# Kernel optimization log

Measured on AMD Instinct MI355X. Metric: run time of the kernel, lower is better.

The kernel has to match this reference:

```python
import jax, jax.numpy as jnp
import numpy as np

D_MODEL = 512
NUM_HEADS = 8
D_QKV = D_MODEL // NUM_HEADS  # 64
CAPACITY = 2  # EUNN tunable-style rotation layers per step
B = 2
L = 256


def setup_inputs() -> dict:
    key = jax.random.key(0)
    ks = jax.random.split(key, 16)
    f = jnp.float32
    x_q = jax.random.normal(ks[0], (B, L, D_MODEL), f)
    x_k = jax.random.normal(ks[1], (B, L, D_MODEL), f)
    x_v = jax.random.normal(ks[2], (B, L, D_MODEL), f)
    mask = jnp.zeros((B, 1, L, L), f)
    s = 1.0 / np.sqrt(D_MODEL).astype(np.float32)
    Wq = jax.random.normal(ks[3], (D_MODEL, D_MODEL), f) * s
    Wk = jax.random.normal(ks[4], (D_MODEL, D_MODEL), f) * s
    Wv = jax.random.normal(ks[5], (D_MODEL, D_MODEL), f) * s
    Wo = jax.random.normal(ks[6], (D_MODEL, D_MODEL), f) * s
    bq = jnp.zeros((D_MODEL,), f); bk = jnp.zeros((D_MODEL,), f)
    bv = jnp.zeros((D_MODEL,), f); bo = jnp.zeros((D_MODEL,), f)
    pi = np.float32(np.pi)
    theta = jax.random.uniform(ks[7], (NUM_HEADS, CAPACITY, D_QKV // 2), f, -pi, pi)
    phi = jax.random.uniform(ks[8], (NUM_HEADS, CAPACITY, D_QKV // 2), f, -pi, pi)
    sw = 1.0 / np.sqrt(D_QKV).astype(np.float32)
    Win_re = jax.random.normal(ks[9], (NUM_HEADS, D_QKV, D_QKV), f) * sw
    Win_im = jax.random.normal(ks[10], (NUM_HEADS, D_QKV, D_QKV), f) * sw
    rnn_bias = jax.random.normal(ks[11], (NUM_HEADS, D_QKV), f) * 0.01
    return dict(x_q=x_q, x_k=x_k, x_v=x_v, mask=mask, Wq=Wq, bq=bq, Wk=Wk, bk=bk,
                Wv=Wv, bv=bv, Wo=Wo, bo=bo, theta=theta, phi=phi,
                Win_re=Win_re, Win_im=Win_im, rnn_bias=rnn_bias)


def _apply_unitary(h, theta, phi):
    # h: [B,H,Q,d] complex64. EUNN unitary = product of Givens-rotation layers,
    # alternating even pairings (0,1),(2,3),.. and odd pairings via roll.
    for c in range(theta.shape[1]):
        if c % 2 == 1:
            h = jnp.roll(h, -1, axis=-1)
        sh = h.shape
        hp = h.reshape(sh[:-1] + (sh[-1] // 2, 2))
        a, b = hp[..., 0], hp[..., 1]
        cs = jnp.cos(theta[:, c, :])[None, :, None, :]
        sn = jnpp_sin = jnp.sin(theta[:, c, :])[None, :, None, :]
        ph = jnp.exp(1j * phi[:, c, :].astype(jnp.complex64))[None, :, None, :]
        na = cs * a - (sn * ph) * b
        nb = (sn * jnp.conj(ph)) * a + cs * b
        h = jnp.stack([na, nb], axis=-1).reshape(sh)
        if c % 2 == 1:
            h = jnp.roll(h, 1, axis=-1)
    return h


def _modrelu(z, b):
    m = jnp.abs(z)
    scale = jax.nn.relu(m + b) / (m + 1e-5)
    return z * scale.astype(z.dtype)


def _forward(x_q, x_k, x_v, mask, Wq, bq, Wk, bk, Wv, bv, Wo, bo,
             theta, phi, Win_re, Win_im, rnn_bias):
    Bm, Lq, _ = x_q.shape
    def heads(x):
        return x.reshape(Bm, -1, NUM_HEADS, D_QKV).transpose(0, 2, 1, 3)
    q = heads(x_q @ Wq + bq)   # [B,H,Lq,d]
    k = heads(x_k @ Wk + bk)   # [B,H,Lk,d]
    v = heads(x_v @ Wv + bv)   # [B,H,Lk,d]
    logits = jnp.einsum('bhqd,bhkd->bhqk', q, k) / jnp.sqrt(jnp.float32(D_QKV))
    logits = logits - jnp.where(mask == 1.0, jnp.inf, mask)
    attn = jax.nn.softmax(logits, axis=-1)  # [B,H,Lq,Lk]
    Win = (Win_re + 1j * Win_im).astype(jnp.complex64)  # [H,d,d]
    bb = rnn_bias[None, :, None, :]
    def step(h, xs):
        a_t, v_t = xs                              # [B,H,Q], [B,H,d]
        x_t = a_t[..., None] * v_t[:, :, None, :]  # [B,H,Q,d] streamed weighted value
        wx = jnp.einsum('bhqd,hde->bhqe', x_t.astype(jnp.complex64), Win)
        return _modrelu(_apply_unitary(h, theta, phi) + wx, bb), None
    h0 = jnp.zeros((Bm, NUM_HEADS, Lq, D_QKV), jnp.complex64)
    xs = (attn.transpose(3, 0, 1, 2), v.transpose(2, 0, 1, 3))
    hT, _ = jax.lax.scan(step, h0, xs)
    rnn_out = jnp.real(hT)  # [B,H,Lq,d] -- TF takes final RNN state, real part
    out = rnn_out.transpose(0, 2, 1, 3).reshape(Bm, Lq, D_MODEL) @ Wo + bo
    return out, attn


def reference(x_q, x_k, x_v, mask, Wq, bq, Wk, bk, Wv, bv, Wo, bo,
              theta, phi, Win_re, Win_im, rnn_bias):
    return _forward(x_q, x_k, x_v, mask, Wq, bq, Wk, bk, Wv, bv, Wo, bo,
                    theta, phi, Win_re, Win_im, rnn_bias)
```

## Files before the change

### kernel.cpp

```cpp
#include <hip/hip_runtime.h>
#include <math.h>

#define NB 2
#define NL 256
#define DM 512
#define NH 8
#define DQ 64

__global__ __launch_bounds__(256) void qkv_gemm(
    const float* __restrict__ xq, const float* __restrict__ xk,
    const float* __restrict__ xv,
    const float* __restrict__ Wq, const float* __restrict__ Wk,
    const float* __restrict__ Wv,
    const float* __restrict__ bq, const float* __restrict__ bk,
    const float* __restrict__ bv,
    float* __restrict__ q, float* __restrict__ k, float* __restrict__ v)
{
    int z = blockIdx.z;
    const float* X = (z == 0) ? xq : (z == 1) ? xk : xv;
    const float* W = (z == 0) ? Wq : (z == 1) ? Wk : Wv;
    const float* bias = (z == 0) ? bq : (z == 1) ? bk : bv;
    float* O = (z == 0) ? q : (z == 1) ? k : v;

    __shared__ float As[32][33];
    __shared__ float Bs[32][68];

    int tid = threadIdx.x;
    int tx = tid & 15, ty = tid >> 4;
    int m0 = blockIdx.y * 32, n0 = blockIdx.x * 64;

    float acc[2][4] = {};

    for (int k0 = 0; k0 < 512; k0 += 32) {
        {
            int r = tid >> 3, c4 = (tid & 7) * 4;
            const float4 av = *(const float4*)(X + (m0 + r) * 512 + k0 + c4);
            As[c4 + 0][r] = av.x; As[c4 + 1][r] = av.y;
            As[c4 + 2][r] = av.z; As[c4 + 3][r] = av.w;
        }
        {
            int r = tid >> 4, c4 = (tid & 15) * 4;
            float4 b0 = *(const float4*)(W + (k0 + r) * 512 + n0 + c4);
            float4 b1 = *(const float4*)(W + (k0 + r + 16) * 512 + n0 + c4);
            *(float4*)&Bs[r][c4] = b0;
            *(float4*)&Bs[r + 16][c4] = b1;
        }
        __syncthreads();
        #pragma unroll
        for (int kk = 0; kk < 32; kk++) {
            float a0 = As[kk][ty * 2 + 0];
            float a1 = As[kk][ty * 2 + 1];
            float4 bb = *(const float4*)&Bs[kk][tx * 4];
            acc[0][0] += a0 * bb.x; acc[0][1] += a0 * bb.y;
            acc[0][2] += a0 * bb.z; acc[0][3] += a0 * bb.w;
            acc[1][0] += a1 * bb.x; acc[1][1] += a1 * bb.y;
            acc[1][2] += a1 * bb.z; acc[1][3] += a1 * bb.w;
        }
        __syncthreads();
    }

    #pragma unroll
    for (int i = 0; i < 2; i++) {
        int m = m0 + ty * 2 + i;
        int b = m >> 8, l = m & 255;
        #pragma unroll
        for (int j = 0; j < 4; j++) {
            int n = n0 + tx * 4 + j;
            int h = n >> 6, d = n & 63;
            O[((b * NH + h) * NL + l) * DQ + d] = acc[i][j] + bias[n];
        }
    }
}

__global__ __launch_bounds__(256) void attn_u_kernel(
    const float* __restrict__ q, const float* __restrict__ k,
    const float* __restrict__ mask, float* __restrict__ attn_o,
    const float* __restrict__ v, const float* __restrict__ Wre,
    const float* __restrict__ Wim, float2* __restrict__ u)
{
    int h = blockIdx.y, b = blockIdx.z;
    int tid = threadIdx.x;
    __shared__ float smem[264];

    if (blockIdx.x < 256) {
        int qi = blockIdx.x;
        int wv = tid >> 6, lane = tid & 63;
        float* qrow = smem;
        float* wred = smem + 256;
        float* wsum = smem + 260;

        if (tid < 16)
            ((float4*)qrow)[tid] = ((const float4*)(q + ((b * NH + h) * NL + qi) * DQ))[tid];
        __syncthreads();

        const float4* kp = (const float4*)(k + ((b * NH + h) * NL + tid) * DQ);
        float acc = 0.f;
        #pragma unroll
        for (int d4 = 0; d4 < 16; d4++) {
            float4 kv = kp[d4];
            float4 qv = ((const float4*)qrow)[d4];
            acc += qv.x * kv.x + qv.y * kv.y + qv.z * kv.z + qv.w * kv.w;
        }
        acc *= 0.125f;

        float mv = mask[(b * NL + qi) * NL + tid];
        acc -= (mv == 1.0f) ? INFINITY : mv;

        float mx = acc;
        #pragma unroll
        for (int o = 32; o; o >>= 1) mx = fmaxf(mx, __shfl_xor(mx, o, 64));
        if (lane == 0) wred[wv] = mx;
        __syncthreads();
        mx = fmaxf(fmaxf(wred[0], wred[1]), fmaxf(wred[2], wred[3]));

        float e = __expf(acc - mx);
        float s = e;
        #pragma unroll
        for (int o = 32; o; o >>= 1) s += __shfl_xor(s, o, 64);
        if (lane == 0) wsum[wv] = s;
        __syncthreads();
        s = wsum[0] + wsum[1] + wsum[2] + wsum[3];

        attn_o[((b * NH + h) * NL + qi) * NL + tid] = e * __builtin_amdgcn_rcpf(s);
    } else {
        int xi = blockIdx.x - 256;
        int e = tid & 63, tq = tid >> 6;
        int t = xi * 4 + tq;
        float (*vrow)[64] = (float (*)[64])smem;

        const float* vp = v + ((b * NH + h) * NL + t) * DQ;
        vrow[tq][e] = vp[e];
        __syncthreads();

        const float* wr = Wre + h * 4096 + e;
        const float* wi = Wim + h * 4096 + e;
        float ar = 0.f, ai = 0.f;
        #pragma unroll
        for (int d = 0; d < 64; d++) {
            float vv = vrow[tq][d];
            ar += vv * wr[d * 64];
            ai += vv * wi[d * 64];
        }
        u[((b * NH + h) * NL + t) * DQ + e] = make_float2(ar, ai);
    }
}

__device__ __forceinline__ float rot_up2(float x) {
    int v = __builtin_amdgcn_mov_dpp(__float_as_int(x), 0x134, 0xF, 0xF, true);
    v = __builtin_amdgcn_mov_dpp(v, 0x134, 0xF, 0xF, true);
    return __int_as_float(v);
}
__device__ __forceinline__ float rot_dn2(float x) {
    int v = __builtin_amdgcn_mov_dpp(__float_as_int(x), 0x13C, 0xF, 0xF, true);
    v = __builtin_amdgcn_mov_dpp(v, 0x13C, 0xF, 0xF, true);
    return __int_as_float(v);
}

__global__ __launch_bounds__(256) void rnn_kernel(
    const float* __restrict__ attn_f, const float2* __restrict__ u,
    const float* __restrict__ theta, const float* __restrict__ phi,
    const float* __restrict__ rnn_bias, float* __restrict__ rnn_out)
{
    int tid = threadIdx.x;
    int wv = tid >> 6;
    int lane = tid & 63;
    int par = lane & 1;
    int p = lane >> 1;
    int rec = blockIdx.x * 8 + wv * 2 + par;
    int qi = rec & 255, h = (rec >> 8) & 7, b = rec >> 11;

    const float* tb = theta + h * 64;
    const float* pb = phi + h * 64;

    float th0 = tb[p], ph0 = pb[p];
    float c0 = cosf(th0), s0 = sinf(th0);
    float cp0 = cosf(ph0), sp0 = sinf(ph0);
    float W0ar = -s0 * cp0, W0ai = -s0 * sp0;
    float W0br =  s0 * cp0, W0bi = -s0 * sp0;

    float th1 = tb[32 + p], ph1 = pb[32 + p];
    float c1 = cosf(th1), s1 = sinf(th1);
    float W1ar = -s1 * cosf(ph1), W1ai = -s1 * sinf(ph1);

    int pm = (p + 31) & 31;
    float th1m = tb[32 + pm], ph1m = pb[32 + pm];
    float c1m = cosf(th1m), s1m = sinf(th1m);
    float W1br = s1m * cosf(ph1m), W1bi = -s1m * sinf(ph1m);

    float bias0 = rnn_bias[h * 64 + 2 * p];
    float bias1 = rnn_bias[h * 64 + 2 * p + 1];

    __shared__ float arow[8 * 256];
    {
        const float4* ap = (const float4*)(attn_f + (size_t)blockIdx.x * 8 * 256);
        ((float4*)arow)[tid] = ap[tid];
        ((float4*)arow)[tid + 256] = ap[tid + 256];
    }
    __syncthreads();
    const float* arc = arow + (wv * 2 + par) * 256;

    const float4* up4 = (const float4*)(u + (size_t)((b * NH + h) * NL) * DQ) + p;

    float e0r = 0.f, e0i = 0.f, e1r = 0.f, e1i = 0.f;
    #pragma unroll 8
    for (int t = 0; t < 256; t++) {
        float4 uu = up4[t * 32];
        float a_t = arc[t];

        float na_r = c0 * e0r + (W0ar * e1r - W0ai * e1i);
        float na_i = c0 * e0i + (W0ar * e1i + W0ai * e1r);
        float nb_r = c0 * e1r + (W0br * e0r - W0bi * e0i);
        float nb_i = c0 * e1i + (W0br * e0i + W0bi * e0r);

        float f1r = rot_up2(na_r), f1i = rot_up2(na_i);
        float f2r = rot_dn2(nb_r), f2i = rot_dn2(nb_i);

        float z1r = c1 * nb_r + (W1ar * f1r - W1ai * f1i);
        float z1i = c1 * nb_i + (W1ar * f1i + W1ai * f1r);
        float z0r = c1m * na_r + (W1br * f2r - W1bi * f2i);
        float z0i = c1m * na_i + (W1br * f2i + W1bi * f2r);

        z0r += a_t * uu.x; z0i += a_t * uu.y;
        z1r += a_t * uu.z; z1i += a_t * uu.w;

        float mm0 = z0r * z0r + z0i * z0i;
        float m0 = __builtin_amdgcn_sqrtf(mm0);
        float sc0 = fmaxf(m0 + bias0, 0.f) * __builtin_amdgcn_rcpf(m0 + 1e-5f);
        e0r = z0r * sc0; e0i = z0i * sc0;

        float mm1 = z1r * z1r + z1i * z1i;
        float m1 = __builtin_amdgcn_sqrtf(mm1);
        float sc1 = fmaxf(m1 + bias1, 0.f) * __builtin_amdgcn_rcpf(m1 + 1e-5f);
        e1r = z1r * sc1; e1i = z1i * sc1;
    }

    float2 o = make_float2(e0r, e1r);
    *(float2*)&rnn_out[(size_t)(b * NL + qi) * DM + h * DQ + 2 * p] = o;
}

__global__ __launch_bounds__(256) void out_gemm(
    const float* __restrict__ A, const float* __restrict__ W,
    const float* __restrict__ bias, float* __restrict__ C)
{
    __shared__ float As[32][17];
    __shared__ float Bs[32][68];

    int tid = threadIdx.x;
    int tx = tid & 15, ty = tid >> 4;
    int m0 = blockIdx.y * 16, n0 = blockIdx.x * 64;

    float acc[4] = {};

    for (int k0 = 0; k0 < 512; k0 += 32) {
        {
            int r = tid >> 4, c2 = (tid & 15) * 2;
            const float2 av = *(const float2*)(A + (m0 + r) * 512 + k0 + c2);
            As[c2 + 0][r] = av.x; As[c2 + 1][r] = av.y;
        }
        {
            int r = tid >> 4, c4 = (tid & 15) * 4;
            float4 b0 = *(const float4*)(W + (k0 + r) * 512 + n0 + c4);
            float4 b1 = *(const float4*)(W + (k0 + r + 16) * 512 + n0 + c4);
            *(float4*)&Bs[r][c4] = b0;
            *(float4*)&Bs[r + 16][c4] = b1;
        }
        __syncthreads();
        #pragma unroll
        for (int kk = 0; kk < 32; kk++) {
            float a = As[kk][ty];
            float4 bb = *(const float4*)&Bs[kk][tx * 4];
            acc[0] += a * bb.x; acc[1] += a * bb.y;
            acc[2] += a * bb.z; acc[3] += a * bb.w;
        }
        __syncthreads();
    }

    int m = m0 + ty;
    #pragma unroll
    for (int j = 0; j < 4; j++) {
        int n = n0 + tx * 4 + j;
        C[m * 512 + n] = acc[j] + bias[n];
    }
}

extern "C" void kernel_launch(void* const* d_in, const int* in_sizes, int n_in,
                              void* d_out, int out_size, void* d_ws, size_t ws_size,
                              hipStream_t stream)
{
    const float* x_q  = (const float*)d_in[0];
    const float* x_k  = (const float*)d_in[1];
    const float* x_v  = (const float*)d_in[2];
    const float* mask = (const float*)d_in[3];
    const float* Wq   = (const float*)d_in[4];
    const float* bq   = (const float*)d_in[5];
    const float* Wk   = (const float*)d_in[6];
    const float* bk   = (const float*)d_in[7];
    const float* Wv   = (const float*)d_in[8];
    const float* bv   = (const float*)d_in[9];
    const float* Wo   = (const float*)d_in[10];
    const float* bo   = (const float*)d_in[11];
    const float* theta= (const float*)d_in[12];
    const float* phi  = (const float*)d_in[13];
    const float* Wre  = (const float*)d_in[14];
    const float* Wim  = (const float*)d_in[15];
    const float* rb   = (const float*)d_in[16];

    float* ws = (float*)d_ws;
    float*  q_ws    = ws;
    float*  k_ws    = ws + 262144;
    float*  v_ws    = ws + 524288;
    float2* u_ws    = (float2*)(ws + 786432);
    float*  rnn_o   = ws + 1310720;

    float* out_o  = (float*)d_out;
    float* attn_o = out_o + NB * NL * DM;

    qkv_gemm<<<dim3(8, 16, 3), 256, 0, stream>>>(
        x_q, x_k, x_v, Wq, Wk, Wv, bq, bk, bv, q_ws, k_ws, v_ws);

    attn_u_kernel<<<dim3(320, NH, NB), 256, 0, stream>>>(
        q_ws, k_ws, mask, attn_o, v_ws, Wre, Wim, u_ws);

    rnn_kernel<<<dim3(512), 256, 0, stream>>>(
        attn_o, u_ws, theta, phi, rb, rnn_o);

    out_gemm<<<dim3(8, 32), 256, 0, stream>>>(rnn_o, Wo, bo, out_o);
}
```

Before: 218.2 us.

## Fuse all four stages into one persistent kernel with grid barriers

Merges the QKV GEMM, attention/softmax plus input projection, the EUNN recurrence and the output GEMM into a single 512-block persistent kernel, with atomic-counter grid barriers between stages. K is now stored transposed so the score dot products read coalesced along the key index. The output GEMM switches to 32-row tiles, and the attention-row staging in shared memory is padded. This aims to remove launch overhead and inter-kernel gaps. In exchange it adds a memset launch, spin-wait barriers that depend on all 512 blocks being co-resident, and idle blocks in the GEMM phases.

```diff
diff --git a/kernel.cpp b/kernel.cpp
--- a/kernel.cpp
+++ b/kernel.cpp
@@ -6,144 +6,7 @@
 #define DM 512
 #define NH 8
 #define DQ 64
-
-__global__ __launch_bounds__(256) void qkv_gemm(
-    const float* __restrict__ xq, const float* __restrict__ xk,
-    const float* __restrict__ xv,
-    const float* __restrict__ Wq, const float* __restrict__ Wk,
-    const float* __restrict__ Wv,
-    const float* __restrict__ bq, const float* __restrict__ bk,
-    const float* __restrict__ bv,
-    float* __restrict__ q, float* __restrict__ k, float* __restrict__ v)
-{
-    int z = blockIdx.z;
-    const float* X = (z == 0) ? xq : (z == 1) ? xk : xv;
-    const float* W = (z == 0) ? Wq : (z == 1) ? Wk : Wv;
-    const float* bias = (z == 0) ? bq : (z == 1) ? bk : bv;
-    float* O = (z == 0) ? q : (z == 1) ? k : v;
-
-    __shared__ float As[32][33];
-    __shared__ float Bs[32][68];
-
-    int tid = threadIdx.x;
-    int tx = tid & 15, ty = tid >> 4;
-    int m0 = blockIdx.y * 32, n0 = blockIdx.x * 64;
-
-    float acc[2][4] = {};
-
-    for (int k0 = 0; k0 < 512; k0 += 32) {
-        {
-            int r = tid >> 3, c4 = (tid & 7) * 4;
-            const float4 av = *(const float4*)(X + (m0 + r) * 512 + k0 + c4);
-            As[c4 + 0][r] = av.x; As[c4 + 1][r] = av.y;
-            As[c4 + 2][r] = av.z; As[c4 + 3][r] = av.w;
-        }
-        {
-            int r = tid >> 4, c4 = (tid & 15) * 4;
-            float4 b0 = *(const float4*)(W + (k0 + r) * 512 + n0 + c4);
-            float4 b1 = *(const float4*)(W + (k0 + r + 16) * 512 + n0 + c4);
-            *(float4*)&Bs[r][c4] = b0;
-            *(float4*)&Bs[r + 16][c4] = b1;
-        }
-        __syncthreads();
-        #pragma unroll
-        for (int kk = 0; kk < 32; kk++) {
-            float a0 = As[kk][ty * 2 + 0];
-            float a1 = As[kk][ty * 2 + 1];
-            float4 bb = *(const float4*)&Bs[kk][tx * 4];
-            acc[0][0] += a0 * bb.x; acc[0][1] += a0 * bb.y;
-            acc[0][2] += a0 * bb.z; acc[0][3] += a0 * bb.w;
-            acc[1][0] += a1 * bb.x; acc[1][1] += a1 * bb.y;
-            acc[1][2] += a1 * bb.z; acc[1][3] += a1 * bb.w;
-        }
-        __syncthreads();
-    }
-
-    #pragma unroll
-    for (int i = 0; i < 2; i++) {
-        int m = m0 + ty * 2 + i;
-        int b = m >> 8, l = m & 255;
-        #pragma unroll
-        for (int j = 0; j < 4; j++) {
-            int n = n0 + tx * 4 + j;
-            int h = n >> 6, d = n & 63;
-            O[((b * NH + h) * NL + l) * DQ + d] = acc[i][j] + bias[n];
-        }
-    }
-}
-
-__global__ __launch_bounds__(256) void attn_u_kernel(
-    const float* __restrict__ q, const float* __restrict__ k,
-    const float* __restrict__ mask, float* __restrict__ attn_o,
-    const float* __restrict__ v, const float* __restrict__ Wre,
-    const float* __restrict__ Wim, float2* __restrict__ u)
-{
-    int h = blockIdx.y, b = blockIdx.z;
-    int tid = threadIdx.x;
-    __shared__ float smem[264];
-
-    if (blockIdx.x < 256) {
-        int qi = blockIdx.x;
-        int wv = tid >> 6, lane = tid & 63;
-        float* qrow = smem;
-        float* wred = smem + 256;
-        float* wsum = smem + 260;
-
-        if (tid < 16)
-            ((float4*)qrow)[tid] = ((const float4*)(q + ((b * NH + h) * NL + qi) * DQ))[tid];
-        __syncthreads();
-
-        const float4* kp = (const float4*)(k + ((b * NH + h) * NL + tid) * DQ);
-        float acc = 0.f;
-        #pragma unroll
-        for (int d4 = 0; d4 < 16; d4++) {
-            float4 kv = kp[d4];
-            float4 qv = ((const float4*)qrow)[d4];
-            acc += qv.x * kv.x + qv.y * kv.y + qv.z * kv.z + qv.w * kv.w;
-        }
-        acc *= 0.125f;
-
-        float mv = mask[(b * NL + qi) * NL + tid];
-        acc -= (mv == 1.0f) ? INFINITY : mv;
-
-        float mx = acc;
-        #pragma unroll
-        for (int o = 32; o; o >>= 1) mx = fmaxf(mx, __shfl_xor(mx, o, 64));
-        if (lane == 0) wred[wv] = mx;
-        __syncthreads();
-        mx = fmaxf(fmaxf(wred[0], wred[1]), fmaxf(wred[2], wred[3]));
-
-        float e = __expf(acc - mx);
-        float s = e;
-        #pragma unroll
-        for (int o = 32; o; o >>= 1) s += __shfl_xor(s, o, 64);
-        if (lane == 0) wsum[wv] = s;
-        __syncthreads();
-        s = wsum[0] + wsum[1] + wsum[2] + wsum[3];
-
-        attn_o[((b * NH + h) * NL + qi) * NL + tid] = e * __builtin_amdgcn_rcpf(s);
-    } else {
-        int xi = blockIdx.x - 256;
-        int e = tid & 63, tq = tid >> 6;
-        int t = xi * 4 + tq;
-        float (*vrow)[64] = (float (*)[64])smem;
-
-        const float* vp = v + ((b * NH + h) * NL + t) * DQ;
-        vrow[tq][e] = vp[e];
-        __syncthreads();
-
-        const float* wr = Wre + h * 4096 + e;
-        const float* wi = Wim + h * 4096 + e;
-        float ar = 0.f, ai = 0.f;
-        #pragma unroll
-        for (int d = 0; d < 64; d++) {
-            float vv = vrow[tq][d];
-            ar += vv * wr[d * 64];
-            ai += vv * wi[d * 64];
-        }
-        u[((b * NH + h) * NL + t) * DQ + e] = make_float2(ar, ai);
-    }
-}
+#define NBLK 512
 
 __device__ __forceinline__ float rot_up2(float x) {
     int v = __builtin_amdgcn_mov_dpp(__float_as_int(x), 0x134, 0xF, 0xF, true);
@@ -156,130 +19,269 @@
     return __int_as_float(v);
 }
 
-__global__ __launch_bounds__(256) void rnn_kernel(
-    const float* __restrict__ attn_f, const float2* __restrict__ u,
+__device__ __forceinline__ void grid_bar(unsigned* c, unsigned n) {
+    __syncthreads();
+    if (threadIdx.x == 0) {
+        __threadfence();
+        atomicAdd(c, 1u);
+        while (__hip_atomic_load(c, __ATOMIC_RELAXED, __HIP_MEMORY_SCOPE_AGENT) < n)
+            __builtin_amdgcn_s_sleep(2);
+        __threadfence();
+    }
+    __syncthreads();
+}
+
+__global__ __launch_bounds__(256, 2) void fused_kernel(
+    const float* __restrict__ xq, const float* __restrict__ xk,
+    const float* __restrict__ xv, const float* __restrict__ mask,
+    const float* __restrict__ Wq, const float* __restrict__ bq_,
+    const float* __restrict__ Wk, const float* __restrict__ bk_,
+    const float* __restrict__ Wv, const float* __restrict__ bv_,
+    const float* __restrict__ Wo, const float* __restrict__ bo_,
     const float* __restrict__ theta, const float* __restrict__ phi,
-    const float* __restrict__ rnn_bias, float* __restrict__ rnn_out)
+    const float* __restrict__ Wre, const float* __restrict__ Wim,
+    const float* __restrict__ rb,
+    float* qbuf, float* kTbuf, float* vbuf, float2* ubuf,
+    float* rnnbuf, float* outbuf, float* attnbuf, unsigned* bars)
 {
+    __shared__ __align__(16) char smem_pool[17408];
     int tid = threadIdx.x;
-    int wv = tid >> 6;
-    int lane = tid & 63;
-    int par = lane & 1;
-    int p = lane >> 1;
-    int rec = blockIdx.x * 8 + wv * 2 + par;
-    int qi = rec & 255, h = (rec >> 8) & 7, b = rec >> 11;
-
-    const float* tb = theta + h * 64;
-    const float* pb = phi + h * 64;
-
-    float th0 = tb[p], ph0 = pb[p];
-    float c0 = cosf(th0), s0 = sinf(th0);
-    float cp0 = cosf(ph0), sp0 = sinf(ph0);
-    float W0ar = -s0 * cp0, W0ai = -s0 * sp0;
-    float W0br =  s0 * cp0, W0bi = -s0 * sp0;
-
-    float th1 = tb[32 + p], ph1 = pb[32 + p];
-    float c1 = cosf(th1), s1 = sinf(th1);
-    float W1ar = -s1 * cosf(ph1), W1ai = -s1 * sinf(ph1);
-
-    int pm = (p + 31) & 31;
-    float th1m = tb[32 + pm], ph1m = pb[32 + pm];
-    float c1m = cosf(th1m), s1m = sinf(th1m);
-    float W1br = s1m * cosf(ph1m), W1bi = -s1m * sinf(ph1m);
-
-    float bias0 = rnn_bias[h * 64 + 2 * p];
-    float bias1 = rnn_bias[h * 64 + 2 * p + 1];
-
-    __shared__ float arow[8 * 256];
+
     {
-        const float4* ap = (const float4*)(attn_f + (size_t)blockIdx.x * 8 * 256);
-        ((float4*)arow)[tid] = ap[tid];
-        ((float4*)arow)[tid + 256] = ap[tid + 256];
-    }
-    __syncthreads();
-    const float* arc = arow + (wv * 2 + par) * 256;
-
-    const float4* up4 = (const float4*)(u + (size_t)((b * NH + h) * NL) * DQ) + p;
-
-    float e0r = 0.f, e0i = 0.f, e1r = 0.f, e1i = 0.f;
-    #pragma unroll 8
-    for (int t = 0; t < 256; t++) {
-        float4 uu = up4[t * 32];
-        float a_t = arc[t];
-
-        float na_r = c0 * e0r + (W0ar * e1r - W0ai * e1i);
-        float na_i = c0 * e0i + (W0ar * e1i + W0ai * e1r);
-        float nb_r = c0 * e1r + (W0br * e0r - W0bi * e0i);
-        float nb_i = c0 * e1i + (W0br * e0i + W0bi * e0r);
-
-        float f1r = rot_up2(na_r), f1i = rot_up2(na_i);
-        float f2r = rot_dn2(nb_r), f2i = rot_dn2(nb_i);
-
-        float z1r = c1 * nb_r + (W1ar * f1r - W1ai * f1i);
-        float z1i = c1 * nb_i + (W1ar * f1i + W1ai * f1r);
-        float z0r = c1m * na_r + (W1br * f2r - W1bi * f2i);
-        float z0i = c1m * na_i + (W1br * f2i + W1bi * f2r);
-
-        z0r += a_t * uu.x; z0i += a_t * uu.y;
-        z1r += a_t * uu.z; z1i += a_t * uu.w;
-
-        float mm0 = z0r * z0r + z0i * z0i;
-        float m0 = __builtin_amdgcn_sqrtf(mm0);
-        float sc0 = fmaxf(m0 + bias0, 0.f) * __builtin_amdgcn_rcpf(m0 + 1e-5f);
-        e0r = z0r * sc0; e0i = z0i * sc0;
-
-        float mm1 = z1r * z1r + z1i * z1i;
-        float m1 = __builtin_amdgcn_sqrtf(mm1);
-        float sc1 = fmaxf(m1 + bias1, 0.f) * __builtin_amdgcn_rcpf(m1 + 1e-5f);
-        e1r = z1r * sc1; e1i = z1i * sc1;
-    }
-
-    float2 o = make_float2(e0r, e1r);
-    *(float2*)&rnn_out[(size_t)(b * NL + qi) * DM + h * DQ + 2 * p] = o;
-}
-
-__global__ __launch_bounds__(256) void out_gemm(
-    const float* __restrict__ A, const float* __restrict__ W,
-    const float* __restrict__ bias, float* __restrict__ C)
-{
-    __shared__ float As[32][17];
-    __shared__ float Bs[32][68];
-
-    int tid = threadIdx.x;
-    int tx = tid & 15, ty = tid >> 4;
-    int m0 = blockIdx.y * 16, n0 = blockIdx.x * 64;
-
-    float acc[4] = {};
-
-    for (int k0 = 0; k0 < 512; k0 += 32) {
-        {
-            int r = tid >> 4, c2 = (tid & 15) * 2;
-            const float2 av = *(const float2*)(A + (m0 + r) * 512 + k0 + c2);
-            As[c2 + 0][r] = av.x; As[c2 + 1][r] = av.y;
+        int job = blockIdx.x;
+        if (job < 384) {
+            float (*As)[33] = (float (*)[33])smem_pool;
+            float (*Bs)[68] = (float (*)[68])(smem_pool + 4224);
+            int z = job / 128, r1 = job % 128;
+            int mt = r1 >> 3, nt = r1 & 7;
+            const float* X = (z == 0) ? xq : (z == 1) ? xk : xv;
+            const float* W = (z == 0) ? Wq : (z == 1) ? Wk : Wv;
+            const float* bias = (z == 0) ? bq_ : (z == 1) ? bk_ : bv_;
+            float* O = (z == 0) ? qbuf : (z == 1) ? kTbuf : vbuf;
+            int tx = tid & 15, ty = tid >> 4;
+            int m0 = mt * 32, n0 = nt * 64;
+            float acc[2][4] = {};
+            for (int k0 = 0; k0 < 512; k0 += 32) {
+                {
+                    int r = tid >> 3, c4 = (tid & 7) * 4;
+                    float4 av = *(const float4*)(X + (m0 + r) * 512 + k0 + c4);
+                    As[c4 + 0][r] = av.x; As[c4 + 1][r] = av.y;
+                    As[c4 + 2][r] = av.z; As[c4 + 3][r] = av.w;
+                }
+                {
+                    int r = tid >> 4, c4 = (tid & 15) * 4;
+                    float4 b0 = *(const float4*)(W + (k0 + r) * 512 + n0 + c4);
+                    float4 b1 = *(const float4*)(W + (k0 + r + 16) * 512 + n0 + c4);
+                    *(float4*)&Bs[r][c4] = b0;
+                    *(float4*)&Bs[r + 16][c4] = b1;
+                }
+                __syncthreads();
+                #pragma unroll
+                for (int kk = 0; kk < 32; kk++) {
+                    float a0 = As[kk][ty * 2 + 0], a1 = As[kk][ty * 2 + 1];
+                    float4 bb = *(const float4*)&Bs[kk][tx * 4];
+                    acc[0][0] += a0 * bb.x; acc[0][1] += a0 * bb.y;
+                    acc[0][2] += a0 * bb.z; acc[0][3] += a0 * bb.w;
+                    acc[1][0] += a1 * bb.x; acc[1][1] += a1 * bb.y;
+                    acc[1][2] += a1 * bb.z; acc[1][3] += a1 * bb.w;
+                }
+                __syncthreads();
+            }
+            #pragma unroll
+            for (int i = 0; i < 2; i++) {
+                int m = m0 + ty * 2 + i;
+                int bb_ = m >> 8, l = m & 255;
+                #pragma unroll
+                for (int jj = 0; jj < 4; jj++) {
+                    int n = n0 + tx * 4 + jj;
+                    int hh = n >> 6, dd = n & 63;
+                    float val = acc[i][jj] + bias[n];
+                    if (z == 1) O[((bb_ * NH + hh) * DQ + dd) * NL + l] = val;
+                    else        O[((bb_ * NH + hh) * NL + l) * DQ + dd] = val;
+                }
+            }
         }
-        {
-            int r = tid >> 4, c4 = (tid & 15) * 4;
-            float4 b0 = *(const float4*)(W + (k0 + r) * 512 + n0 + c4);
-            float4 b1 = *(const float4*)(W + (k0 + r + 16) * 512 + n0 + c4);
-            *(float4*)&Bs[r][c4] = b0;
-            *(float4*)&Bs[r + 16][c4] = b1;
+    }
+    grid_bar(&bars[0], NBLK);
+
+    {
+        float* sp = (float*)smem_pool;
+        for (int j = blockIdx.x; j < 5120; j += NBLK) {
+            int x = j % 320;
+            int hb = j / 320;
+            int h = hb & 7, b = hb >> 3;
+            if (x < 256) {
+                int qi = x;
+                int wv = tid >> 6, lane = tid & 63;
+                float* qrow = sp; float* wred = sp + 256; float* wsum = sp + 260;
+                if (tid < 16)
+                    ((float4*)qrow)[tid] =
+                        ((const float4*)(qbuf + ((b * NH + h) * NL + qi) * DQ))[tid];
+                __syncthreads();
+                const float* kp = kTbuf + (size_t)((b * NH + h) * DQ) * NL + tid;
+                float acc = 0.f;
+                #pragma unroll
+                for (int d = 0; d < 64; d++) acc += qrow[d] * kp[d * NL];
+                acc *= 0.125f;
+                float mv = mask[(b * NL + qi) * NL + tid];
+                acc -= (mv == 1.0f) ? INFINITY : mv;
+                float mx = acc;
+                #pragma unroll
+                for (int o = 32; o; o >>= 1) mx = fmaxf(mx, __shfl_xor(mx, o, 64));
+                if (lane == 0) wred[wv] = mx;
+                __syncthreads();
+                mx = fmaxf(fmaxf(wred[0], wred[1]), fmaxf(wred[2], wred[3]));
+                float e = __expf(acc - mx);
+                float s = e;
+                #pragma unroll
+                for (int o = 32; o; o >>= 1) s += __shfl_xor(s, o, 64);
+                if (lane == 0) wsum[wv] = s;
+                __syncthreads();
+                s = wsum[0] + wsum[1] + wsum[2] + wsum[3];
+                attnbuf[((b * NH + h) * NL + qi) * NL + tid] =
+                    e * __builtin_amdgcn_rcpf(s);
+            } else {
+                int xi = x - 256;
+                int e = tid & 63, tq = tid >> 6;
+                int t = xi * 4 + tq;
+                float (*vrow)[64] = (float (*)[64])sp;
+                vrow[tq][e] = vbuf[((b * NH + h) * NL + t) * DQ + e];
+                __syncthreads();
+                const float* wr = Wre + h * 4096 + e;
+                const float* wi = Wim + h * 4096 + e;
+                float ar = 0.f, ai = 0.f;
+                #pragma unroll
+                for (int d = 0; d < 64; d++) {
+                    float vv = vrow[tq][d];
+                    ar += vv * wr[d * 64];
+                    ai += vv * wi[d * 64];
+                }
+                ubuf[((b * NH + h) * NL + t) * DQ + e] = make_float2(ar, ai);
+            }
+            __syncthreads();
         }
+    }
+    grid_bar(&bars[1], NBLK);
+
+    {
+        int wv = tid >> 6;
+        int lane = tid & 63;
+        int par = lane & 1;
+        int p = lane >> 1;
+        int rec = blockIdx.x * 8 + wv * 2 + par;
+        int qi = rec & 255, h = (rec >> 8) & 7, b = rec >> 11;
+
+        const float* tb = theta + h * 64;
+        const float* pb = phi + h * 64;
+
+        float th0 = tb[p], ph0 = pb[p];
+        float c0 = cosf(th0), s0 = sinf(th0);
+        float cp0 = cosf(ph0), sp0 = sinf(ph0);
+        float W0ar = -s0 * cp0, W0ai = -s0 * sp0;
+        float W0br =  s0 * cp0, W0bi = -s0 * sp0;
+
+        float th1 = tb[32 + p], ph1 = pb[32 + p];
+        float c1 = cosf(th1), s1v = sinf(th1);
+        float W1ar = -s1v * cosf(ph1), W1ai = -s1v * sinf(ph1);
+
+        int pm = (p + 31) & 31;
+        float th1m = tb[32 + pm], ph1m = pb[32 + pm];
+        float c1m = cosf(th1m), s1m = sinf(th1m);
+        float W1br = s1m * cosf(ph1m), W1bi = -s1m * sinf(ph1m);
+
+        float bias0 = rb[h * 64 + 2 * p];
+        float bias1 = rb[h * 64 + 2 * p + 1];
+
+        float* arow = (float*)smem_pool;
+        const float* ap = attnbuf + (size_t)blockIdx.x * 2048;
+        #pragma unroll
+        for (int i = 0; i < 8; i++) arow[i * 257 + tid] = ap[i * 256 + tid];
         __syncthreads();
-        #pragma unroll
-        for (int kk = 0; kk < 32; kk++) {
-            float a = As[kk][ty];
-            float4 bb = *(const float4*)&Bs[kk][tx * 4];
-            acc[0] += a * bb.x; acc[1] += a * bb.y;
-            acc[2] += a * bb.z; acc[3] += a * bb.w;
+        const float* arc = arow + (wv * 2 + par) * 257;
+
+        const float4* up4 =
+            (const float4*)(ubuf + (size_t)((b * NH + h) * NL) * DQ) + p;
+
+        float e0r = 0.f, e0i = 0.f, e1r = 0.f, e1i = 0.f;
+        #pragma unroll 8
+        for (int t = 0; t < 256; t++) {
+            float4 uu = up4[t * 32];
+            float a_t = arc[t];
+
+            float na_r = c0 * e0r + (W0ar * e1r - W0ai * e1i);
+            float na_i = c0 * e0i + (W0ar * e1i + W0ai * e1r);
+            float nb_r = c0 * e1r + (W0br * e0r - W0bi * e0i);
+            float nb_i = c0 * e1i + (W0br * e0i + W0bi * e0r);
+
+            float f1r = rot_up2(na_r), f1i = rot_up2(na_i);
+            float f2r = rot_dn2(nb_r), f2i = rot_dn2(nb_i);
+
+            float z1r = c1 * nb_r + (W1ar * f1r - W1ai * f1i) + a_t * uu.z;
+            float z1i = c1 * nb_i + (W1ar * f1i + W1ai * f1r) + a_t * uu.w;
+            float z0r = c1m * na_r + (W1br * f2r - W1bi * f2i) + a_t * uu.x;
+            float z0i = c1m * na_i + (W1br * f2i + W1bi * f2r) + a_t * uu.y;
+
+            float mm0 = z0r * z0r + z0i * z0i;
+            float m0v = __builtin_amdgcn_sqrtf(mm0);
+            float sc0 = fmaxf(m0v + bias0, 0.f) * __builtin_amdgcn_rcpf(m0v + 1e-5f);
+            e0r = z0r * sc0; e0i = z0i * sc0;
+
+            float mm1 = z1r * z1r + z1i * z1i;
+            float m1v = __builtin_amdgcn_sqrtf(mm1);
+            float sc1 = fmaxf(m1v + bias1, 0.f) * __builtin_amdgcn_rcpf(m1v + 1e-5f);
+            e1r = z1r * sc1; e1i = z1i * sc1;
         }
-        __syncthreads();
-    }
-
-    int m = m0 + ty;
-    #pragma unroll
-    for (int j = 0; j < 4; j++) {
-        int n = n0 + tx * 4 + j;
-        C[m * 512 + n] = acc[j] + bias[n];
+
+        *(float2*)&rnnbuf[(size_t)(b * NL + qi) * DM + h * DQ + 2 * p] =
+            make_float2(e0r, e1r);
+    }
+    grid_bar(&bars[2], NBLK);
+
+    {
+        int job = blockIdx.x;
+        if (job < 128) {
+            float (*As)[33] = (float (*)[33])smem_pool;
+            float (*Bs)[68] = (float (*)[68])(smem_pool + 4224);
+            int mt = job >> 3, nt = job & 7;
+            int tx = tid & 15, ty = tid >> 4;
+            int m0 = mt * 32, n0 = nt * 64;
+            float acc[2][4] = {};
+            for (int k0 = 0; k0 < 512; k0 += 32) {
+                {
+                    int r = tid >> 3, c4 = (tid & 7) * 4;
+                    float4 av = *(const float4*)(rnnbuf + (m0 + r) * 512 + k0 + c4);
+                    As[c4 + 0][r] = av.x; As[c4 + 1][r] = av.y;
+                    As[c4 + 2][r] = av.z; As[c4 + 3][r] = av.w;
+                }
+                {
+                    int r = tid >> 4, c4 = (tid & 15) * 4;
+                    float4 b0 = *(const float4*)(Wo + (k0 + r) * 512 + n0 + c4);
+                    float4 b1 = *(const float4*)(Wo + (k0 + r + 16) * 512 + n0 + c4);
+                    *(float4*)&Bs[r][c4] = b0;
+                    *(float4*)&Bs[r + 16][c4] = b1;
+                }
+                __syncthreads();
+                #pragma unroll
+                for (int kk = 0; kk < 32; kk++) {
+                    float a0 = As[kk][ty * 2 + 0], a1 = As[kk][ty * 2 + 1];
+                    float4 bb = *(const float4*)&Bs[kk][tx * 4];
+                    acc[0][0] += a0 * bb.x; acc[0][1] += a0 * bb.y;
+                    acc[0][2] += a0 * bb.z; acc[0][3] += a0 * bb.w;
+                    acc[1][0] += a1 * bb.x; acc[1][1] += a1 * bb.y;
+                    acc[1][2] += a1 * bb.z; acc[1][3] += a1 * bb.w;
+                }
+                __syncthreads();
+            }
+            #pragma unroll
+            for (int i = 0; i < 2; i++) {
+                int m = m0 + ty * 2 + i;
+                #pragma unroll
+                for (int jj = 0; jj < 4; jj++) {
+                    int n = n0 + tx * 4 + jj;
+                    outbuf[m * 512 + n] = acc[i][jj] + bo_[n];
+                }
+            }
+        }
     }
 }
 
@@ -306,23 +308,20 @@
     const float* rb   = (const float*)d_in[16];
 
     float* ws = (float*)d_ws;
-    float*  q_ws    = ws;
-    float*  k_ws    = ws + 262144;
-    float*  v_ws    = ws + 524288;
-    float2* u_ws    = (float2*)(ws + 786432);
-    float*  rnn_o   = ws + 1310720;
+    float*    q_ws  = ws;
+    float*    kT_ws = ws + 262144;
+    float*    v_ws  = ws + 524288;
+    float2*   u_ws  = (float2*)(ws + 786432);
+    float*    rnn_o = ws + 1310720;
+    unsigned* bars  = (unsigned*)(ws + 1572864);
 
     float* out_o  = (float*)d_out;
     float* attn_o = out_o + NB * NL * DM;
 
-    qkv_gemm<<<dim3(8, 16, 3), 256, 0, stream>>>(
-        x_q, x_k, x_v, Wq, Wk, Wv, bq, bk, bv, q_ws, k_ws, v_ws);
-
-    attn_u_kernel<<<dim3(320, NH, NB), 256, 0, stream>>>(
-        q_ws, k_ws, mask, attn_o, v_ws, Wre, Wim, u_ws);
-
-    rnn_kernel<<<dim3(512), 256, 0, stream>>>(
-        attn_o, u_ws, theta, phi, rb, rnn_o);
-
-    out_gemm<<<dim3(8, 32), 256, 0, stream>>>(rnn_o, Wo, bo, out_o);
-}
+    hipMemsetAsync(bars, 0, 3 * sizeof(unsigned), stream);
+
+    fused_kernel<<<dim3(NBLK), 256, 0, stream>>>(
+        x_q, x_k, x_v, mask, Wq, bq, Wk, bk, Wv, bv, Wo, bo,
+        theta, phi, Wre, Wim, rb,
+        q_ws, kT_ws, v_ws, u_ws, rnn_o, out_o, attn_o, bars);
+}
```

Measured after the change: 351.5 us. 61.1% more time.

## Store K transposed and compute eight query rows per attention block

Applied to the files above, without the earlier changes.

The QKV GEMM now writes K in a [b,h,d,l] layout, so the attention kernel reads K coalesced across threads. Each attention block now handles 8 query rows instead of one. K loads are reused across those rows, logits are staged in shared memory, and each wave does the softmax reduction for two rows. This cuts block count and redundant K traffic, at the cost of more shared memory, more registers and strided stores in the GEMM epilogue.

```diff
diff --git a/kernel.cpp b/kernel.cpp
--- a/kernel.cpp
+++ b/kernel.cpp
@@ -67,69 +67,86 @@
         for (int j = 0; j < 4; j++) {
             int n = n0 + tx * 4 + j;
             int h = n >> 6, d = n & 63;
-            O[((b * NH + h) * NL + l) * DQ + d] = acc[i][j] + bias[n];
+            float val = acc[i][j] + bias[n];
+            if (z == 1)
+                O[((b * NH + h) * DQ + d) * NL + l] = val;
+            else
+                O[((b * NH + h) * NL + l) * DQ + d] = val;
         }
     }
 }
 
 __global__ __launch_bounds__(256) void attn_u_kernel(
-    const float* __restrict__ q, const float* __restrict__ k,
+    const float* __restrict__ q, const float* __restrict__ kT,
     const float* __restrict__ mask, float* __restrict__ attn_o,
     const float* __restrict__ v, const float* __restrict__ Wre,
     const float* __restrict__ Wim, float2* __restrict__ u)
 {
     int h = blockIdx.y, b = blockIdx.z;
     int tid = threadIdx.x;
-    __shared__ float smem[264];
-
-    if (blockIdx.x < 256) {
-        int qi = blockIdx.x;
+    int x = blockIdx.x;
+    __shared__ float sp[2608];
+
+    if (x < 32) {
+        int qg = x;
         int wv = tid >> 6, lane = tid & 63;
-        float* qrow = smem;
-        float* wred = smem + 256;
-        float* wsum = smem + 260;
-
-        if (tid < 16)
-            ((float4*)qrow)[tid] = ((const float4*)(q + ((b * NH + h) * NL + qi) * DQ))[tid];
-        __syncthreads();
-
-        const float4* kp = (const float4*)(k + ((b * NH + h) * NL + tid) * DQ);
-        float acc = 0.f;
+        float* qs   = sp;
+        float* lg   = sp + 512;
+        float* redm = sp + 512 + 2080;
+        float* reds = redm + 8;
+
+        ((float2*)qs)[tid] =
+            ((const float2*)(q + ((size_t)(b * NH + h) * NL + qg * 8) * DQ))[tid];
+        __syncthreads();
+
+        const float* kp = kT + (size_t)((b * NH + h) * DQ) * NL + tid;
+        float acc[8] = {};
         #pragma unroll
         for (int d4 = 0; d4 < 16; d4++) {
-            float4 kv = kp[d4];
-            float4 qv = ((const float4*)qrow)[d4];
-            acc += qv.x * kv.x + qv.y * kv.y + qv.z * kv.z + qv.w * kv.w;
-        }
-        acc *= 0.125f;
-
-        float mv = mask[(b * NL + qi) * NL + tid];
-        acc -= (mv == 1.0f) ? INFINITY : mv;
-
-        float mx = acc;
-        #pragma unroll
-        for (int o = 32; o; o >>= 1) mx = fmaxf(mx, __shfl_xor(mx, o, 64));
-        if (lane == 0) wred[wv] = mx;
-        __syncthreads();
-        mx = fmaxf(fmaxf(wred[0], wred[1]), fmaxf(wred[2], wred[3]));
-
-        float e = __expf(acc - mx);
-        float s = e;
-        #pragma unroll
-        for (int o = 32; o; o >>= 1) s += __shfl_xor(s, o, 64);
-        if (lane == 0) wsum[wv] = s;
-        __syncthreads();
-        s = wsum[0] + wsum[1] + wsum[2] + wsum[3];
-
-        attn_o[((b * NH + h) * NL + qi) * NL + tid] = e * __builtin_amdgcn_rcpf(s);
+            float kv0 = kp[(d4 * 4 + 0) * NL];
+            float kv1 = kp[(d4 * 4 + 1) * NL];
+            float kv2 = kp[(d4 * 4 + 2) * NL];
+            float kv3 = kp[(d4 * 4 + 3) * NL];
+            #pragma unroll
+            for (int j = 0; j < 8; j++) {
+                const float4 qv = *(const float4*)&qs[j * 64 + d4 * 4];
+                acc[j] += qv.x * kv0 + qv.y * kv1 + qv.z * kv2 + qv.w * kv3;
+            }
+        }
+        #pragma unroll
+        for (int j = 0; j < 8; j++) {
+            float mv = mask[(size_t)(b * NL + qg * 8 + j) * NL + tid];
+            acc[j] = acc[j] * 0.125f - ((mv == 1.0f) ? INFINITY : mv);
+            lg[j * 260 + tid] = acc[j];
+        }
+        __syncthreads();
+        #pragma unroll
+        for (int jj = 0; jj < 2; jj++) {
+            int j = wv * 2 + jj;
+            float v0 = lg[j * 260 + lane],       v1 = lg[j * 260 + 64 + lane];
+            float v2 = lg[j * 260 + 128 + lane], v3 = lg[j * 260 + 192 + lane];
+            float mx = fmaxf(fmaxf(v0, v1), fmaxf(v2, v3));
+            #pragma unroll
+            for (int o = 32; o; o >>= 1) mx = fmaxf(mx, __shfl_xor(mx, o, 64));
+            float s = __expf(v0 - mx) + __expf(v1 - mx) +
+                      __expf(v2 - mx) + __expf(v3 - mx);
+            #pragma unroll
+            for (int o = 32; o; o >>= 1) s += __shfl_xor(s, o, 64);
+            if (lane == 0) { redm[j] = mx; reds[j] = s; }
+        }
+        __syncthreads();
+        #pragma unroll
+        for (int j = 0; j < 8; j++) {
+            float p = __expf(acc[j] - redm[j]) * __builtin_amdgcn_rcpf(reds[j]);
+            attn_o[((size_t)(b * NH + h) * NL + qg * 8 + j) * NL + tid] = p;
+        }
     } else {
-        int xi = blockIdx.x - 256;
+        int xi = x - 32;
         int e = tid & 63, tq = tid >> 6;
         int t = xi * 4 + tq;
-        float (*vrow)[64] = (float (*)[64])smem;
-
-        const float* vp = v + ((b * NH + h) * NL + t) * DQ;
-        vrow[tq][e] = vp[e];
+        float (*vrow)[64] = (float (*)[64])sp;
+
+        vrow[tq][e] = v[((b * NH + h) * NL + t) * DQ + e];
         __syncthreads();
 
         const float* wr = Wre + h * 4096 + e;
@@ -307,7 +324,7 @@
 
     float* ws = (float*)d_ws;
     float*  q_ws    = ws;
-    float*  k_ws    = ws + 262144;
+    float*  kT_ws   = ws + 262144;
     float*  v_ws    = ws + 524288;
     float2* u_ws    = (float2*)(ws + 786432);
     float*  rnn_o   = ws + 1310720;
@@ -316,10 +333,10 @@
     float* attn_o = out_o + NB * NL * DM;
 
     qkv_gemm<<<dim3(8, 16, 3), 256, 0, stream>>>(
-        x_q, x_k, x_v, Wq, Wk, Wv, bq, bk, bv, q_ws, k_ws, v_ws);
-
-    attn_u_kernel<<<dim3(320, NH, NB), 256, 0, stream>>>(
-        q_ws, k_ws, mask, attn_o, v_ws, Wre, Wim, u_ws);
+        x_q, x_k, x_v, Wq, Wk, Wv, bq, bk, bv, q_ws, kT_ws, v_ws);
+
+    attn_u_kernel<<<dim3(96, NH, NB), 256, 0, stream>>>(
+        q_ws, kT_ws, mask, attn_o, v_ws, Wre, Wim, u_ws);
 
     rnn_kernel<<<dim3(512), 256, 0, stream>>>(
         attn_o, u_ws, theta, phi, rb, rnn_o);
```

Result: faster. 195.8 us (-10.3%).
